# Kernel tuning notes

Hardware: AMD Instinct MI355X
Metric: run time of the kernel (lower is better)

The kernel has to match this reference:

```python
import jax, jax.numpy as jnp
import numpy as np

N = 100_000          # nodes
E = 3_200_000        # edges (avg degree 32)
NODE_DIM = 46        # expanded_dim_node (first 5 cols = node-type one-hot)
EDGE_DIM = 65        # edge_attr dim; message dim = EDGE_DIM - 1 = 64
EMB = 128            # conv MLP output dim
HID_FFN = 64
B = 16               # graphs in batch
C = 2                # num_classes
NEG = -1e30
THREAD_ONEHOT = np.array([0., 0., 0., 0., 1.], dtype=np.float32)


def setup_inputs() -> dict:
    key = jax.random.key(0)
    ks = jax.random.split(key, 10)
    x = jax.random.uniform(ks[0], (N, NODE_DIM), dtype=jnp.float32)
    # make every 4th node a thread-node ([0,0,0,0,1]); others [1,0,0,0,0]
    is_thread = (jnp.arange(N) % 4 == 0)
    nodetype = jnp.where(is_thread[:, None],
                         jnp.asarray(THREAD_ONEHOT),
                         jnp.asarray([1., 0., 0., 0., 0.], dtype=jnp.float32))
    x = x.at[:, :5].set(nodetype)
    edge_index = jax.random.randint(ks[1], (2, E), 0, N, dtype=jnp.int64)
    edge_attr = jax.random.uniform(ks[2], (E, EDGE_DIM), dtype=jnp.float32)
    ptr = jnp.arange(0, N + 1, N // B, dtype=jnp.int64)  # [B+1], equal-size graphs
    s = 0.05
    W1 = jax.random.normal(ks[3], (EDGE_DIM - 1, EMB), dtype=jnp.float32) * s
    b1 = jnp.zeros((EMB,), dtype=jnp.float32)
    W2 = jax.random.normal(ks[4], (EMB, EMB), dtype=jnp.float32) * s
    b2 = jnp.zeros((EMB,), dtype=jnp.float32)
    Wf1 = jax.random.normal(ks[5], (EMB, HID_FFN), dtype=jnp.float32) * s
    bf1 = jnp.zeros((HID_FFN,), dtype=jnp.float32)
    Wf2 = jax.random.normal(ks[6], (HID_FFN, C), dtype=jnp.float32) * s
    bf2 = jnp.zeros((C,), dtype=jnp.float32)
    return {"x": x, "edge_index": edge_index, "edge_attr": edge_attr, "ptr": ptr,
            "W1": W1, "b1": b1, "W2": W2, "b2": b2,
            "Wf1": Wf1, "bf1": bf1, "Wf2": Wf2, "bf2": bf2}


def reference(x, edge_index, edge_attr, ptr, W1, b1, W2, b2, Wf1, bf1, Wf2, bf2):
    n = x.shape[0]
    n_graphs = ptr.shape[0] - 1
    # message: edge_attr[:, :-1]; aggregate: scatter-add into target nodes
    msg = edge_attr[:, :-1]                                        # [E, 64]
    agg = jax.ops.segment_sum(msg, edge_index[1], num_segments=n)  # [N, 64]
    # h_Theta MLP applied to aggregated node features
    h = jnp.dot(jax.nn.relu(jnp.dot(agg, W1) + b1), W2) + b2       # [N, EMB]
    # thread-node mask: x[:, :5] == [0,0,0,0,1]
    thread_mask = jnp.all(x[:, :5] == jnp.asarray(THREAD_ONEHOT), axis=1)  # [N]
    # batch id per node: bucketize(node_idx, ptr, right=True) - 1
    batch = jnp.searchsorted(ptr, jnp.arange(n, dtype=ptr.dtype), side='right') - 1
    # global max pool over thread nodes per graph
    h_masked = jnp.where(thread_mask[:, None], h, NEG)
    pooled = jax.ops.segment_max(h_masked, batch, num_segments=n_graphs)  # [B, EMB]
    # FFN classifier head
    logits = jnp.dot(jax.nn.relu(jnp.dot(pooled, Wf1) + bf1), Wf2) + bf2  # [B, C]
    return logits
```

## Files before the change

kernel.cpp:

```cpp
#include <hip/hip_runtime.h>

#define NEGV -1.0e30f
#define CAP 128

__device__ __forceinline__ float rl(float v, int l) {
  return __int_as_float(__builtin_amdgcn_readlane(__float_as_int(v), l));
}

__device__ __forceinline__ void atomicMaxF(float* addr, float v) {
  if (v >= 0.0f) atomicMax((int*)addr, __float_as_int(v));
  else atomicMin((unsigned int*)addr, __float_as_uint(v));
}

__global__ __launch_bounds__(256) void k_prep(
    const float* __restrict__ x, const int* __restrict__ ptr,
    int n, int nptr, int* __restrict__ mask, int* __restrict__ batch,
    int* __restrict__ rank, int* __restrict__ nodeof, int* __restrict__ deg,
    int* __restrict__ cnt, float* __restrict__ pooled, int npooled) {
  int i = blockIdx.x * blockDim.x + threadIdx.x;
  if (i < npooled) pooled[i] = NEGV;
  if (i >= n) return;
  const float* xr = x + (long long)i * 46;
  bool m = (xr[0] == 0.0f) && (xr[1] == 0.0f) && (xr[2] == 0.0f) &&
           (xr[3] == 0.0f) && (xr[4] == 1.0f);
  mask[i] = m ? 1 : 0;
  if (m) {
    int r = atomicAdd(cnt, 1);
    rank[i] = r;
    nodeof[r] = i;
    deg[r] = 0;
  }
  int b = 0;
  for (int g = 1; g < nptr; ++g)
    if (i >= ptr[g]) b = g;
  batch[i] = b;
}

__global__ __launch_bounds__(256) void k_fill(
    const int* __restrict__ ei, const int* __restrict__ mask,
    const int* __restrict__ rank, int* __restrict__ deg,
    int* __restrict__ elist, long long E) {
  long long e = (long long)blockIdx.x * blockDim.x + threadIdx.x;
  if (e >= E) return;
  int dst = __builtin_nontemporal_load(ei + E + e);
  if (mask[dst] == 0) return;
  int r = rank[dst];
  int pos = atomicAdd(&deg[r], 1);
  if (pos < CAP) elist[(size_t)r * CAP + pos] = (int)e;
}

__global__ __launch_bounds__(256) void k_gather(
    const float* __restrict__ ea, const int* __restrict__ nodeof,
    const int* __restrict__ deg, const int* __restrict__ elist,
    const int* __restrict__ cnt, float* __restrict__ agg, int n) {
  const int t = blockIdx.x * blockDim.x + threadIdx.x;
  const int wv = t >> 6;
  const int lane = t & 63;
  if (wv >= cnt[0]) return;
  const int node = nodeof[wv];
  int d = deg[wv];
  d = min(d, CAP);
  const int* el = elist + (size_t)wv * CAP;
  float acc = 0.0f;
  int k = 0;
  for (; k + 8 <= d; k += 8) {
    const int4 ia = *(const int4*)(el + k);
    const int4 ib = *(const int4*)(el + k + 4);
    const float v0 = __builtin_nontemporal_load(ea + (long long)ia.x * 65 + lane);
    const float v1 = __builtin_nontemporal_load(ea + (long long)ia.y * 65 + lane);
    const float v2 = __builtin_nontemporal_load(ea + (long long)ia.z * 65 + lane);
    const float v3 = __builtin_nontemporal_load(ea + (long long)ia.w * 65 + lane);
    const float v4 = __builtin_nontemporal_load(ea + (long long)ib.x * 65 + lane);
    const float v5 = __builtin_nontemporal_load(ea + (long long)ib.y * 65 + lane);
    const float v6 = __builtin_nontemporal_load(ea + (long long)ib.z * 65 + lane);
    const float v7 = __builtin_nontemporal_load(ea + (long long)ib.w * 65 + lane);
    acc += ((v0 + v1) + (v2 + v3)) + ((v4 + v5) + (v6 + v7));
  }
  for (; k < d; ++k)
    acc += __builtin_nontemporal_load(ea + (long long)el[k] * 65 + lane);
  agg[(size_t)node * 64 + lane] = acc;
}

__global__ __launch_bounds__(256) void k_mlp(
    const float* __restrict__ agg, const int* __restrict__ mask,
    const int* __restrict__ batch,
    const float* __restrict__ W1, const float* __restrict__ b1,
    const float* __restrict__ W2, const float* __restrict__ b2,
    float* __restrict__ pooled, int n) {
  const int lane = threadIdx.x & 63;
  const int wv = blockIdx.x * 4 + (threadIdx.x >> 6);
  const int n0 = wv * 16;
  if (n0 >= n) return;
  const int cnt = min(16, n - n0);
  int mv = 0, bvv = 0;
  if (lane < cnt) {
    mv = mask[n0 + lane];
    bvv = batch[n0 + lane];
  }
  unsigned long long bal = __ballot(mv != 0);
  unsigned mb = (unsigned)(bal & 0xFFFFull);
  if (mb == 0) return;

  const float bias1a = b1[lane], bias1b = b1[64 + lane];
  const float bias2a = b2[lane], bias2b = b2[64 + lane];
  float m0 = NEGV, m1 = NEGV;
  int cur = -1;

  while (mb) {
    int nd[4];
    int lastid = 0;
#pragma unroll
    for (int s = 0; s < 4; ++s) {
      if (mb) { lastid = __ffs(mb) - 1; mb &= mb - 1; }
      nd[s] = lastid;
    }
    float a[4], t0[4], t1[4];
#pragma unroll
    for (int s = 0; s < 4; ++s) {
      a[s] = agg[(size_t)(n0 + nd[s]) * 64 + lane];
      t0[s] = bias1a;
      t1[s] = bias1b;
    }
#pragma unroll 16
    for (int l = 0; l < 64; ++l) {
      const float w0 = W1[l * 128 + lane];
      const float w1 = W1[l * 128 + 64 + lane];
#pragma unroll
      for (int s = 0; s < 4; ++s) {
        const float av = rl(a[s], l);
        t0[s] = fmaf(av, w0, t0[s]);
        t1[s] = fmaf(av, w1, t1[s]);
      }
    }
    float h0[4], h1[4];
#pragma unroll
    for (int s = 0; s < 4; ++s) {
      t0[s] = fmaxf(t0[s], 0.0f);
      t1[s] = fmaxf(t1[s], 0.0f);
      h0[s] = bias2a;
      h1[s] = bias2b;
    }
#pragma unroll 16
    for (int j = 0; j < 64; ++j) {
      const float w0 = W2[j * 128 + lane];
      const float w1 = W2[j * 128 + 64 + lane];
      const float w2 = W2[(64 + j) * 128 + lane];
      const float w3 = W2[(64 + j) * 128 + 64 + lane];
#pragma unroll
      for (int s = 0; s < 4; ++s) {
        const float u = rl(t0[s], j);
        const float v = rl(t1[s], j);
        h0[s] = fmaf(u, w0, h0[s]);
        h1[s] = fmaf(u, w1, h1[s]);
        h0[s] = fmaf(v, w2, h0[s]);
        h1[s] = fmaf(v, w3, h1[s]);
      }
    }
#pragma unroll
    for (int s = 0; s < 4; ++s) {
      const int bb = __builtin_amdgcn_readlane(bvv, nd[s]);
      if (bb != cur) {
        if (cur >= 0) {
          atomicMaxF(pooled + cur * 128 + lane, m0);
          atomicMaxF(pooled + cur * 128 + 64 + lane, m1);
        }
        cur = bb;
        m0 = NEGV;
        m1 = NEGV;
      }
      m0 = fmaxf(m0, h0[s]);
      m1 = fmaxf(m1, h1[s]);
    }
  }
  if (cur >= 0) {
    atomicMaxF(pooled + cur * 128 + lane, m0);
    atomicMaxF(pooled + cur * 128 + 64 + lane, m1);
  }
}

__global__ __launch_bounds__(1024) void k_ffn(
    const float* __restrict__ pooled,
    const float* __restrict__ Wf1, const float* __restrict__ bf1,
    const float* __restrict__ Wf2, const float* __restrict__ bf2,
    float* __restrict__ out, int B) {
  __shared__ float hid[1024];
  int t = threadIdx.x;
  if (t < B * 64) {
    int g = t >> 6, j = t & 63;
    float acc = bf1[j];
    for (int k = 0; k < 128; ++k)
      acc = fmaf(pooled[g * 128 + k], Wf1[k * 64 + j], acc);
    hid[t] = fmaxf(acc, 0.0f);
  }
  __syncthreads();
  if (t < B * 2) {
    int g = t >> 1, c = t & 1;
    float acc = bf2[c];
    for (int j = 0; j < 64; ++j)
      acc = fmaf(hid[g * 64 + j], Wf2[j * 2 + c], acc);
    out[t] = acc;
  }
}

extern "C" void kernel_launch(void* const* d_in, const int* in_sizes, int n_in,
                              void* d_out, int out_size, void* d_ws, size_t ws_size,
                              hipStream_t stream) {
  const float* x = (const float*)d_in[0];
  const int* ei = (const int*)d_in[1];
  const float* ea = (const float*)d_in[2];
  const int* ptr = (const int*)d_in[3];
  const float* W1 = (const float*)d_in[4];
  const float* b1 = (const float*)d_in[5];
  const float* W2 = (const float*)d_in[6];
  const float* b2 = (const float*)d_in[7];
  const float* Wf1 = (const float*)d_in[8];
  const float* bf1 = (const float*)d_in[9];
  const float* Wf2 = (const float*)d_in[10];
  const float* bf2 = (const float*)d_in[11];

  const int n = in_sizes[0] / 46;
  const long long E = (long long)in_sizes[1] / 2;
  const int nptr = in_sizes[3];
  const int nB = nptr - 1;

  char* ws = (char*)d_ws;
  float* agg = (float*)ws;
  int* mask = (int*)(ws + (size_t)n * 64 * 4);
  int* batch = mask + n;
  float* pooled = (float*)(batch + n);
  int* rank = (int*)(pooled + (size_t)nB * 128);
  int* nodeof = rank + n;
  int* deg = nodeof + n;
  int* cnt = deg + n;
  int* elist = cnt + 64;

  hipMemsetAsync(cnt, 0, 4, stream);
  k_prep<<<(n + 255) / 256, 256, 0, stream>>>(x, ptr, n, nptr, mask, batch,
                                              rank, nodeof, deg, cnt,
                                              pooled, nB * 128);
  k_fill<<<(int)((E + 255) / 256), 256, 0, stream>>>(ei, mask, rank, deg,
                                                     elist, E);
  k_gather<<<(n * 64 + 255) / 256, 256, 0, stream>>>(ea, nodeof, deg, elist,
                                                     cnt, agg, n);
  const int waves = (n + 15) / 16;
  k_mlp<<<(waves + 3) / 4, 256, 0, stream>>>(agg, mask, batch, W1, b1, W2, b2,
                                             pooled, n);
  k_ffn<<<1, 1024, 0, stream>>>(pooled, Wf1, bf1, Wf2, bf2, (float*)d_out, nB);
}
```

Measured before the change: 209.6 us.

## Fuse gather with MLP and pooling; vectorize edge fill four per thread

After: 271.1 us. 1.29x slower.

```diff
diff --git a/kernel.cpp b/kernel.cpp
--- a/kernel.cpp
+++ b/kernel.cpp
@@ -40,142 +40,82 @@
     const int* __restrict__ ei, const int* __restrict__ mask,
     const int* __restrict__ rank, int* __restrict__ deg,
     int* __restrict__ elist, long long E) {
-  long long e = (long long)blockIdx.x * blockDim.x + threadIdx.x;
-  if (e >= E) return;
-  int dst = __builtin_nontemporal_load(ei + E + e);
-  if (mask[dst] == 0) return;
-  int r = rank[dst];
-  int pos = atomicAdd(&deg[r], 1);
-  if (pos < CAP) elist[(size_t)r * CAP + pos] = (int)e;
+  long long base = ((long long)blockIdx.x * blockDim.x + threadIdx.x) * 4;
+  if (base >= E) return;
+  int dst4[4];
+  if (base + 4 <= E) {
+    const int4 q = *(const int4*)(ei + E + base);
+    dst4[0] = q.x; dst4[1] = q.y; dst4[2] = q.z; dst4[3] = q.w;
+  } else {
+    for (int j = 0; j < 4; ++j)
+      dst4[j] = (base + j < E) ? ei[E + base + j] : -1;
+  }
+#pragma unroll
+  for (int j = 0; j < 4; ++j) {
+    const int dst = dst4[j];
+    if (dst < 0 || (base + j >= E)) continue;
+    if (mask[dst] == 0) continue;
+    const int r = rank[dst];
+    const int pos = atomicAdd(&deg[r], 1);
+    if (pos < CAP) elist[(size_t)r * CAP + pos] = (int)(base + j);
+  }
 }
 
-__global__ __launch_bounds__(256) void k_gather(
+__global__ __launch_bounds__(256) void k_gather_mlp(
     const float* __restrict__ ea, const int* __restrict__ nodeof,
     const int* __restrict__ deg, const int* __restrict__ elist,
-    const int* __restrict__ cnt, float* __restrict__ agg, int n) {
+    const int* __restrict__ cnt, const int* __restrict__ batch,
+    const float* __restrict__ W1, const float* __restrict__ b1,
+    const float* __restrict__ W2, const float* __restrict__ b2,
+    float* __restrict__ pooled) {
   const int t = blockIdx.x * blockDim.x + threadIdx.x;
   const int wv = t >> 6;
   const int lane = t & 63;
   if (wv >= cnt[0]) return;
   const int node = nodeof[wv];
-  int d = deg[wv];
-  d = min(d, CAP);
+  int d = min(deg[wv], CAP);
   const int* el = elist + (size_t)wv * CAP;
+
   float acc = 0.0f;
   int k = 0;
   for (; k + 8 <= d; k += 8) {
     const int4 ia = *(const int4*)(el + k);
     const int4 ib = *(const int4*)(el + k + 4);
-    const float v0 = __builtin_nontemporal_load(ea + (long long)ia.x * 65 + lane);
-    const float v1 = __builtin_nontemporal_load(ea + (long long)ia.y * 65 + lane);
-    const float v2 = __builtin_nontemporal_load(ea + (long long)ia.z * 65 + lane);
-    const float v3 = __builtin_nontemporal_load(ea + (long long)ia.w * 65 + lane);
-    const float v4 = __builtin_nontemporal_load(ea + (long long)ib.x * 65 + lane);
-    const float v5 = __builtin_nontemporal_load(ea + (long long)ib.y * 65 + lane);
-    const float v6 = __builtin_nontemporal_load(ea + (long long)ib.z * 65 + lane);
-    const float v7 = __builtin_nontemporal_load(ea + (long long)ib.w * 65 + lane);
+    const float v0 = ea[(long long)ia.x * 65 + lane];
+    const float v1 = ea[(long long)ia.y * 65 + lane];
+    const float v2 = ea[(long long)ia.z * 65 + lane];
+    const float v3 = ea[(long long)ia.w * 65 + lane];
+    const float v4 = ea[(long long)ib.x * 65 + lane];
+    const float v5 = ea[(long long)ib.y * 65 + lane];
+    const float v6 = ea[(long long)ib.z * 65 + lane];
+    const float v7 = ea[(long long)ib.w * 65 + lane];
     acc += ((v0 + v1) + (v2 + v3)) + ((v4 + v5) + (v6 + v7));
   }
-  for (; k < d; ++k)
-    acc += __builtin_nontemporal_load(ea + (long long)el[k] * 65 + lane);
-  agg[(size_t)node * 64 + lane] = acc;
-}
+  for (; k < d; ++k) acc += ea[(long long)el[k] * 65 + lane];
 
-__global__ __launch_bounds__(256) void k_mlp(
-    const float* __restrict__ agg, const int* __restrict__ mask,
-    const int* __restrict__ batch,
-    const float* __restrict__ W1, const float* __restrict__ b1,
-    const float* __restrict__ W2, const float* __restrict__ b2,
-    float* __restrict__ pooled, int n) {
-  const int lane = threadIdx.x & 63;
-  const int wv = blockIdx.x * 4 + (threadIdx.x >> 6);
-  const int n0 = wv * 16;
-  if (n0 >= n) return;
-  const int cnt = min(16, n - n0);
-  int mv = 0, bvv = 0;
-  if (lane < cnt) {
-    mv = mask[n0 + lane];
-    bvv = batch[n0 + lane];
+  float t0 = b1[lane], t1 = b1[64 + lane];
+#pragma unroll 16
+  for (int l = 0; l < 64; ++l) {
+    const float av = rl(acc, l);
+    t0 = fmaf(av, W1[l * 128 + lane], t0);
+    t1 = fmaf(av, W1[l * 128 + 64 + lane], t1);
   }
-  unsigned long long bal = __ballot(mv != 0);
-  unsigned mb = (unsigned)(bal & 0xFFFFull);
-  if (mb == 0) return;
+  t0 = fmaxf(t0, 0.0f);
+  t1 = fmaxf(t1, 0.0f);
+  float h0 = b2[lane], h1 = b2[64 + lane];
+#pragma unroll 16
+  for (int m = 0; m < 64; ++m) {
+    const float u = rl(t0, m);
+    const float v = rl(t1, m);
+    h0 = fmaf(u, W2[m * 128 + lane], h0);
+    h1 = fmaf(u, W2[m * 128 + 64 + lane], h1);
+    h0 = fmaf(v, W2[(64 + m) * 128 + lane], h0);
+    h1 = fmaf(v, W2[(64 + m) * 128 + 64 + lane], h1);
+  }
 
-  const float bias1a = b1[lane], bias1b = b1[64 + lane];
-  const float bias2a = b2[lane], bias2b = b2[64 + lane];
-  float m0 = NEGV, m1 = NEGV;
-  int cur = -1;
-
-  while (mb) {
-    int nd[4];
-    int lastid = 0;
-#pragma unroll
-    for (int s = 0; s < 4; ++s) {
-      if (mb) { lastid = __ffs(mb) - 1; mb &= mb - 1; }
-      nd[s] = lastid;
-    }
-    float a[4], t0[4], t1[4];
-#pragma unroll
-    for (int s = 0; s < 4; ++s) {
-      a[s] = agg[(size_t)(n0 + nd[s]) * 64 + lane];
-      t0[s] = bias1a;
-      t1[s] = bias1b;
-    }
-#pragma unroll 16
-    for (int l = 0; l < 64; ++l) {
-      const float w0 = W1[l * 128 + lane];
-      const float w1 = W1[l * 128 + 64 + lane];
-#pragma unroll
-      for (int s = 0; s < 4; ++s) {
-        const float av = rl(a[s], l);
-        t0[s] = fmaf(av, w0, t0[s]);
-        t1[s] = fmaf(av, w1, t1[s]);
-      }
-    }
-    float h0[4], h1[4];
-#pragma unroll
-    for (int s = 0; s < 4; ++s) {
-      t0[s] = fmaxf(t0[s], 0.0f);
-      t1[s] = fmaxf(t1[s], 0.0f);
-      h0[s] = bias2a;
-      h1[s] = bias2b;
-    }
-#pragma unroll 16
-    for (int j = 0; j < 64; ++j) {
-      const float w0 = W2[j * 128 + lane];
-      const float w1 = W2[j * 128 + 64 + lane];
-      const float w2 = W2[(64 + j) * 128 + lane];
-      const float w3 = W2[(64 + j) * 128 + 64 + lane];
-#pragma unroll
-      for (int s = 0; s < 4; ++s) {
-        const float u = rl(t0[s], j);
-        const float v = rl(t1[s], j);
-        h0[s] = fmaf(u, w0, h0[s]);
-        h1[s] = fmaf(u, w1, h1[s]);
-        h0[s] = fmaf(v, w2, h0[s]);
-        h1[s] = fmaf(v, w3, h1[s]);
-      }
-    }
-#pragma unroll
-    for (int s = 0; s < 4; ++s) {
-      const int bb = __builtin_amdgcn_readlane(bvv, nd[s]);
-      if (bb != cur) {
-        if (cur >= 0) {
-          atomicMaxF(pooled + cur * 128 + lane, m0);
-          atomicMaxF(pooled + cur * 128 + 64 + lane, m1);
-        }
-        cur = bb;
-        m0 = NEGV;
-        m1 = NEGV;
-      }
-      m0 = fmaxf(m0, h0[s]);
-      m1 = fmaxf(m1, h1[s]);
-    }
-  }
-  if (cur >= 0) {
-    atomicMaxF(pooled + cur * 128 + lane, m0);
-    atomicMaxF(pooled + cur * 128 + 64 + lane, m1);
-  }
+  const int b = batch[node];
+  atomicMaxF(pooled + b * 128 + lane, h0);
+  atomicMaxF(pooled + b * 128 + 64 + lane, h1);
 }
 
 __global__ __launch_bounds__(1024) void k_ffn(
@@ -224,8 +164,7 @@
   const int nB = nptr - 1;
 
   char* ws = (char*)d_ws;
-  float* agg = (float*)ws;
-  int* mask = (int*)(ws + (size_t)n * 64 * 4);
+  int* mask = (int*)ws;
   int* batch = mask + n;
   float* pooled = (float*)(batch + n);
   int* rank = (int*)(pooled + (size_t)nB * 128);
@@ -238,12 +177,9 @@
   k_prep<<<(n + 255) / 256, 256, 0, stream>>>(x, ptr, n, nptr, mask, batch,
                                               rank, nodeof, deg, cnt,
                                               pooled, nB * 128);
-  k_fill<<<(int)((E + 255) / 256), 256, 0, stream>>>(ei, mask, rank, deg,
-                                                     elist, E);
-  k_gather<<<(n * 64 + 255) / 256, 256, 0, stream>>>(ea, nodeof, deg, elist,
-                                                     cnt, agg, n);
-  const int waves = (n + 15) / 16;
-  k_mlp<<<(waves + 3) / 4, 256, 0, stream>>>(agg, mask, batch, W1, b1, W2, b2,
-                                             pooled, n);
+  k_fill<<<(int)((E + 1023) / 1024), 256, 0, stream>>>(ei, mask, rank, deg,
+                                                       elist, E);
+  k_gather_mlp<<<(n * 64 + 255) / 256, 256, 0, stream>>>(
+      ea, nodeof, deg, elist, cnt, batch, W1, b1, W2, b2, pooled);
   k_ffn<<<1, 1024, 0, stream>>>(pooled, Wf1, bf1, Wf2, bf2, (float*)d_out, nB);
 }
```
